# Kernel tuning notes

Hardware: AMD Instinct MI355X
Metric: run time of the kernel (lower is better)

Reference implementation:

```python
import jax, jax.numpy as jnp
import numpy as np

EPS = 1e-5
N_HEAD = 8

def setup_inputs() -> dict:
    key = jax.random.key(0)
    ks = jax.random.split(key, 8)
    n, c, h, w = 8, 512, 64, 64
    feats_in = 512
    x = jax.random.normal(ks[0], (n, c, h, w), jnp.float32)
    cond = jax.random.normal(ks[1], (n, feats_in), jnp.float32)
    # AdaGN linear: feats_in -> 2*c
    W_ada = jax.random.normal(ks[2], (feats_in, 2 * c), jnp.float32) * (1.0 / np.sqrt(feats_in))
    b_ada = jnp.zeros((2 * c,), jnp.float32)
    # qkv 1x1 conv: c -> 3c
    W_qkv = jax.random.normal(ks[3], (3 * c, c), jnp.float32) * (1.0 / np.sqrt(c))
    b_qkv = jnp.zeros((3 * c,), jnp.float32)
    # out 1x1 conv: c -> c
    W_out = jax.random.normal(ks[4], (c, c), jnp.float32) * (1.0 / np.sqrt(c))
    b_out = jnp.zeros((c,), jnp.float32)
    return {"x": x, "cond": cond, "W_ada": W_ada, "b_ada": b_ada,
            "W_qkv": W_qkv, "b_qkv": b_qkv, "W_out": W_out, "b_out": b_out}

def reference(x, cond, W_ada, b_ada, W_qkv, b_qkv, W_out, b_out):
    n, c, h, w = x.shape
    nh = N_HEAD
    dh = c // nh
    s = h * w
    # AdaGN: GroupNorm with 1 group, no affine, then scale/shift from cond
    scales_shifts = cond @ W_ada + b_ada  # [n, 2c]
    scales, shifts = scales_shifts[:, :c], scales_shifts[:, c:]
    xf = x.reshape(n, -1)
    mean = xf.mean(axis=1, keepdims=True)
    var = xf.var(axis=1, keepdims=True)
    normed = ((xf - mean) * jax.lax.rsqrt(var + EPS)).reshape(n, c, h, w)
    normed = shifts[:, :, None, None] + normed * (scales[:, :, None, None] + 1.0)
    # qkv 1x1 conv
    qkv = jnp.einsum('nchw,oc->nohw', normed, W_qkv) + b_qkv[None, :, None, None]
    # view [n, nh*3, dh, s] then transpose -> [n, nh*3, s, dh]
    qkv = qkv.reshape(n, nh * 3, dh, s).transpose(0, 1, 3, 2)
    q, k, v = jnp.split(qkv, 3, axis=1)  # each [n, nh, s, dh]
    scale = dh ** (-0.25)
    att = jnp.einsum('nhsd,nhtd->nhst', q * scale, k * scale)
    att = jax.nn.softmax(att, axis=-1)
    y = jnp.einsum('nhst,nhtd->nhsd', att, v)  # [n, nh, s, dh]
    y = y.transpose(0, 1, 3, 2).reshape(n, c, h, w)
    out = jnp.einsum('nchw,oc->nohw', y, W_out) + b_out[None, :, None, None]
    return x + out
```

## Files before the change

### kernel.cpp

```cpp
#include <hip/hip_runtime.h>

#define NB   8
#define CC   512
#define SS   4096
#define NHD  8
#define DH   64
#define FEAT 512
#define NPER (CC*SS)

typedef unsigned short ushort_t;
typedef __attribute__((ext_vector_type(8))) short bf16x8;
typedef __attribute__((ext_vector_type(4))) float f32x4;

__device__ inline float b2f(ushort_t h) {
    union { unsigned int u; float f; } v; v.u = ((unsigned int)h) << 16; return v.f;
}
__device__ inline ushort_t f2b(float f) {
    union { float f; unsigned int u; } v; v.f = f;
    unsigned int u = v.u;
    u += 0x7fffu + ((u >> 16) & 1u);
    return (ushort_t)(u >> 16);
}
__device__ inline void unpack8(uint4 v, ushort_t* us) {
    us[0] = v.x & 0xffff; us[1] = v.x >> 16;
    us[2] = v.y & 0xffff; us[3] = v.y >> 16;
    us[4] = v.z & 0xffff; us[5] = v.z >> 16;
    us[6] = v.w & 0xffff; us[7] = v.w >> 16;
}
__device__ inline float loadIn(const void* p, size_t idx, int isf) {
    return isf ? ((const float*)p)[idx] : b2f(((const ushort_t*)p)[idx]);
}
__device__ inline void load8(const void* p, size_t idx, int isf, float* f) {
    if (isf) {
        const float* q = (const float*)p + idx;
        float4 a = *(const float4*)q, b = *(const float4*)(q + 4);
        f[0]=a.x; f[1]=a.y; f[2]=a.z; f[3]=a.w; f[4]=b.x; f[5]=b.y; f[6]=b.z; f[7]=b.w;
    } else {
        uint4 v = *(const uint4*)((const ushort_t*)p + idx);
        ushort_t us[8]; unpack8(v, us);
        for (int j = 0; j < 8; ++j) f[j] = b2f(us[j]);
    }
}
__device__ inline bf16x8 loadfrag(const void* p, size_t idx, int isf) {
    if (isf) {
        float f[8]; load8(p, idx, 1, f);
        bf16x8 r;
        for (int j = 0; j < 8; ++j) r[j] = (short)f2b(f[j]);
        return r;
    }
    union { uint4 u; bf16x8 v; } cvt;
    cvt.u = *(const uint4*)((const ushort_t*)p + idx);
    return cvt.v;
}

typedef __attribute__((address_space(1))) const unsigned int gas_u32;
typedef __attribute__((address_space(3))) unsigned int las_u32;
__device__ inline void gload_lds16(const void* g, void* l) {
    __builtin_amdgcn_global_load_lds((gas_u32*)g, (las_u32*)l, 16, 0, 0);
}

__global__ void probe_kernel(const unsigned int* __restrict__ x, int* __restrict__ flag) {
    unsigned int w = x[threadIdx.x & 63];
    unsigned int elo = (w >> 7) & 0xFF;
    int hit = (elo >= 0x60 && elo <= 0x9F) ? 1 : 0;
    for (int m = 1; m < 64; m <<= 1) hit += __shfl_xor(hit, m, 64);
    if (threadIdx.x == 0) *flag = (hit >= 40) ? 0 : 1;
}

__global__ __launch_bounds__(256) void ada_kernel(
    const void* __restrict__ cond, const void* __restrict__ W,
    const void* __restrict__ bias, float* __restrict__ out,
    const int* __restrict__ flagp)
{
    int isf = *flagp;
    int n = blockIdx.x;
    int j = blockIdx.y * 256 + threadIdx.x;
    float acc = loadIn(bias, j, isf);
    for (int k = 0; k < FEAT; ++k)
        acc += loadIn(cond, (size_t)n * FEAT + k, isf) * loadIn(W, (size_t)k * (2 * CC) + j, isf);
    out[n * (2 * CC) + j] = acc;
}

__global__ __launch_bounds__(256) void stats_kernel(
    const void* __restrict__ x, float* __restrict__ part, const int* __restrict__ flagp)
{
    int isf = *flagp;
    int n = blockIdx.x, blk = blockIdx.y;
    int tid = threadIdx.x;
    float s = 0.f, ss = 0.f;
    size_t base8 = (size_t)blk * 4096 + tid;
    for (int i = 0; i < 16; ++i) {
        float f[8];
        load8(x, ((size_t)n * NPER) + (base8 + (size_t)i * 256) * 8, isf, f);
        for (int j = 0; j < 8; ++j) { s += f[j]; ss += f[j] * f[j]; }
    }
    for (int m = 1; m < 64; m <<= 1) { s += __shfl_xor(s, m, 64); ss += __shfl_xor(ss, m, 64); }
    int w = tid >> 6;
    if ((tid & 63) == 0) {
        part[(size_t)n * 512 + (blk * 4 + w) * 2 + 0] = s;
        part[(size_t)n * 512 + (blk * 4 + w) * 2 + 1] = ss;
    }
}

__global__ __launch_bounds__(256) void coef_kernel(
    const float* __restrict__ ada, const float* __restrict__ part,
    float* __restrict__ coefA, float* __restrict__ coefB)
{
    __shared__ float reds[4], redss[4], mv[2];
    int n = blockIdx.x;
    int tid = threadIdx.x;
    float s  = part[(size_t)n * 512 + tid * 2 + 0];
    float ss = part[(size_t)n * 512 + tid * 2 + 1];
    for (int m = 1; m < 64; m <<= 1) { s += __shfl_xor(s, m, 64); ss += __shfl_xor(ss, m, 64); }
    int w = tid >> 6, lane = tid & 63;
    if (lane == 0) { reds[w] = s; redss[w] = ss; }
    __syncthreads();
    if (tid == 0) {
        float S  = (reds[0] + reds[1]) + (reds[2] + reds[3]);
        float S2 = (redss[0] + redss[1]) + (redss[2] + redss[3]);
        float inv = 1.f / (float)NPER;
        float mean = S * inv;
        float var  = S2 * inv - mean * mean;
        mv[0] = mean;
        mv[1] = rsqrtf(var + 1e-5f);
    }
    __syncthreads();
    float mean = mv[0], r = mv[1];
    int c = blockIdx.y * 256 + tid;
    float a = (ada[n * (2 * CC) + c] + 1.f) * r;
    coefA[n * CC + c] = a;
    coefB[n * CC + c] = ada[n * (2 * CC) + CC + c] - mean * a;
}

__global__ __launch_bounds__(256) void qkv_gemm_kernel(
    const void* __restrict__ A, const void* __restrict__ X, const void* __restrict__ bias,
    ushort_t* __restrict__ C,
    const float* __restrict__ coefA, const float* __restrict__ coefB,
    const int* __restrict__ flagp, int nb, int hb, int hc)
{
    __shared__ __align__(16) short Alds[64][72];
    __shared__ __align__(16) short Blds[64][72];
    int isf = *flagp;
    int z = blockIdx.z;
    int nIdx = nb + z;
    int yb = blockIdx.y;
    int p = yb / hc, hh = yb % hc;
    int arow0 = p * 512 + (hb + hh) * 64;
    size_t cbase = ((size_t)(z * 3 + p) * (hc * 64) + hh * 64) * SS;
    int n0 = blockIdx.x * 64;
    int tid = threadIdx.x;
    int w = tid >> 6, lane = tid & 63;
    int quad = lane >> 4, l16 = lane & 15;
    int wm = (w >> 1) * 32, wn = (w & 1) * 32;
    f32x4 acc[2][2] = {};

    for (int k0 = 0; k0 < 512; k0 += 64) {
        __syncthreads();
        for (int it = 0; it < 2; ++it) {
            int chunk = tid + it * 256;
            int row = chunk >> 3, cb = chunk & 7;
            float f[8];
            load8(A, (size_t)(arow0 + row) * 512 + k0 + cb * 8, isf, f);
            short o[8];
            for (int j = 0; j < 8; ++j) o[j] = (short)f2b(f[j]);
            *(uint4*)&Alds[row][cb * 8] = *(uint4*)o;
        }
        for (int it = 0; it < 2; ++it) {
            int chunk = tid + it * 256;
            int c = chunk >> 3, hb8 = chunk & 7;
            int ch = k0 + c;
            float f[8];
            load8(X, (size_t)nIdx * NPER + (size_t)ch * SS + n0 + hb8 * 8, isf, f);
            float a = coefA[nIdx * CC + ch], b = coefB[nIdx * CC + ch];
            for (int j = 0; j < 8; ++j)
                Blds[hb8 * 8 + j][c] = (short)f2b(a * f[j] + b);
        }
        __syncthreads();
        for (int kk = 0; kk < 2; ++kk) {
            bf16x8 af[2], bfv[2];
            for (int mi = 0; mi < 2; ++mi)
                af[mi] = *(const bf16x8*)&Alds[wm + mi * 16 + l16][kk * 32 + quad * 8];
            for (int ni = 0; ni < 2; ++ni)
                bfv[ni] = *(const bf16x8*)&Blds[wn + ni * 16 + l16][kk * 32 + quad * 8];
            for (int mi = 0; mi < 2; ++mi)
                for (int ni = 0; ni < 2; ++ni)
                    acc[mi][ni] = __builtin_amdgcn_mfma_f32_16x16x32_bf16(
                        af[mi], bfv[ni], acc[mi][ni], 0, 0, 0);
        }
    }
    if (p < 2) {
        const float SCL = 0.42467078f;
        for (int mi = 0; mi < 2; ++mi)
            for (int ni = 0; ni < 2; ++ni) {
                int col = n0 + wn + ni * 16 + l16;
                int d0 = wm + mi * 16 + quad * 4;
                ushort_t pk[4];
                for (int r = 0; r < 4; ++r) {
                    float v = (acc[mi][ni][r] + loadIn(bias, arow0 + d0 + r, isf)) * SCL;
                    pk[r] = f2b(v);
                }
                *(ushort4*)&C[cbase + (size_t)col * 64 + d0] =
                    make_ushort4(pk[0], pk[1], pk[2], pk[3]);
            }
    } else {
        for (int mi = 0; mi < 2; ++mi)
            for (int ni = 0; ni < 2; ++ni) {
                int col = n0 + wn + ni * 16 + l16;
                for (int r = 0; r < 4; ++r) {
                    int rowl = wm + mi * 16 + quad * 4 + r;
                    float v = acc[mi][ni][r] + loadIn(bias, arow0 + rowl, isf);
                    C[cbase + (size_t)rowl * SS + col] = f2b(v);
                }
            }
    }
}

__global__ __launch_bounds__(256, 4) void attn_kernel(
    const ushort_t* __restrict__ qkv,
    ushort_t* __restrict__ y,
    int nb, int hb, int hc)
{
    __shared__ __align__(16) short Klds[2][64][64];
    __shared__ __align__(16) short Vlds[2][64][64];

    int s0 = blockIdx.x * 128;
    int hl = blockIdx.y;
    int z = blockIdx.z;
    int n = nb + z;
    int hcc = hc * 64;
    const ushort_t* Q = qkv + ((size_t)(z * 3 + 0) * hcc + hl * 64) * SS;
    const ushort_t* K = qkv + ((size_t)(z * 3 + 1) * hcc + hl * 64) * SS;
    const ushort_t* V = qkv + ((size_t)(z * 3 + 2) * hcc + hl * 64) * SS;

    int tid = threadIdx.x;
    int w = tid >> 6, lane = tid & 63;
    int quad = lane >> 4, l16 = lane & 15;
    int sw = l16 & 7;

    bf16x8 qf[2][2];
    for (int si = 0; si < 2; ++si)
        for (int kk = 0; kk < 2; ++kk)
            qf[si][kk] = *(const bf16x8*)&Q[(size_t)(s0 + w * 32 + si * 16 + l16) * 64
                                            + kk * 32 + quad * 8];

    auto stage = [&](int b, int tt) {
        #pragma unroll
        for (int it = 0; it < 2; ++it) {
            int chunk = it * 256 + tid;
            int row = chunk >> 3;
            int ssl = (chunk & 7) ^ (row & 7);
            int cb0 = it * 256 + w * 64;
            gload_lds16(&K[(size_t)(tt + row) * 64 + ssl * 8], (short*)Klds[b] + cb0 * 8);
            gload_lds16(&V[(size_t)row * SS + tt + ssl * 8],   (short*)Vlds[b] + cb0 * 8);
        }
    };

    const short ONE = 0x3F80;
    bf16x8 ones = { ONE, ONE, ONE, ONE, ONE, ONE, ONE, ONE };

    f32x4 o[2][4] = {};
    f32x4 sum_acc[2] = {};

    stage(0, 0);

    for (int t0 = 0; t0 < SS; t0 += 64) {
        int cur = (t0 >> 6) & 1;
        __syncthreads();
        if (t0 + 64 < SS) stage(cur ^ 1, t0 + 64);

        for (int kk = 0; kk < 2; ++kk) {
            f32x4 sv[2][2];
            for (int ntl = 0; ntl < 2; ++ntl) {
                int nt = kk * 2 + ntl;
                bf16x8 kf0 = *(const bf16x8*)&Klds[cur][nt * 16 + l16][((0 * 4 + quad) ^ sw) * 8];
                bf16x8 kf1 = *(const bf16x8*)&Klds[cur][nt * 16 + l16][((1 * 4 + quad) ^ sw) * 8];
                for (int si = 0; si < 2; ++si) {
                    f32x4 a = { -16.f, -16.f, -16.f, -16.f };
                    a = __builtin_amdgcn_mfma_f32_16x16x32_bf16(kf0, qf[si][0], a, 0, 0, 0);
                    a = __builtin_amdgcn_mfma_f32_16x16x32_bf16(kf1, qf[si][1], a, 0, 0, 0);
                    sv[ntl][si] = a;
                }
            }

            bf16x8 vf[4];
            for (int dt = 0; dt < 4; ++dt)
                vf[dt] = *(const bf16x8*)&Vlds[cur][dt * 16 + l16][((kk * 4 + quad) ^ sw) * 8];

            for (int si = 0; si < 2; ++si) {
                float p0 = exp2f(sv[0][si][0]), p1 = exp2f(sv[0][si][1]);
                float p2 = exp2f(sv[0][si][2]), p3 = exp2f(sv[0][si][3]);
                float p4 = exp2f(sv[1][si][0]), p5 = exp2f(sv[1][si][1]);
                float p6 = exp2f(sv[1][si][2]), p7 = exp2f(sv[1][si][3]);
                unsigned int x0, x1, y0, y1;
                asm("v_cvt_pk_bf16_f32 %0, %1, %2" : "=v"(x0) : "v"(p0), "v"(p1));
                asm("v_cvt_pk_bf16_f32 %0, %1, %2" : "=v"(x1) : "v"(p2), "v"(p3));
                asm("v_cvt_pk_bf16_f32 %0, %1, %2" : "=v"(y0) : "v"(p4), "v"(p5));
                asm("v_cvt_pk_bf16_f32 %0, %1, %2" : "=v"(y1) : "v"(p6), "v"(p7));
                asm("v_permlane32_swap_b32 %0, %1" : "+v"(x0), "+v"(y0));
                asm("v_permlane32_swap_b32 %0, %1" : "+v"(x1), "+v"(y1));
                asm("v_permlane16_swap_b32 %0, %1" : "+v"(x0), "+v"(y0));
                asm("v_permlane16_swap_b32 %0, %1" : "+v"(x1), "+v"(y1));
                union { unsigned int u[4]; bf16x8 v; } frag;
                frag.u[0] = x0; frag.u[1] = x1; frag.u[2] = y0; frag.u[3] = y1;

                sum_acc[si] = __builtin_amdgcn_mfma_f32_16x16x32_bf16(frag.v, ones, sum_acc[si], 0, 0, 0);
                for (int dt = 0; dt < 4; ++dt)
                    o[si][dt] = __builtin_amdgcn_mfma_f32_16x16x32_bf16(frag.v, vf[dt], o[si][dt], 0, 0, 0);
            }
        }
    }

    for (int si = 0; si < 2; ++si) {
        f32x4 inv;
        for (int r = 0; r < 4; ++r) inv[r] = 1.0f / sum_acc[si][r];
        for (int dt = 0; dt < 4; ++dt) {
            int d = dt * 16 + l16;
            int cidx = (hb + hl) * DH + d;
            size_t bidx = ((size_t)n * CC + cidx) * SS + s0 + w * 32 + si * 16 + quad * 4;
            ushort_t pk[4];
            for (int r = 0; r < 4; ++r) pk[r] = f2b(o[si][dt][r] * inv[r]);
            *(ushort4*)&y[bidx] = make_ushort4(pk[0], pk[1], pk[2], pk[3]);
        }
    }
}

__global__ __launch_bounds__(512) void out_gemm_kernel(
    const void* __restrict__ W, const void* __restrict__ bias, const void* __restrict__ x,
    const ushort_t* __restrict__ ybuf, float* __restrict__ out,
    const int* __restrict__ flagp)
{
    __shared__ __align__(16) short Ylds[64][264];
    int isf = *flagp;
    int n = blockIdx.y;
    int s0 = blockIdx.x * 64;
    int tid = threadIdx.x;
    int w = tid >> 6, lane = tid & 63;
    int quad = lane >> 4, l16 = lane & 15;
    const ushort_t* Yb = ybuf + (size_t)n * ((size_t)CC * SS);
    float* Op = out + (size_t)n * NPER;

    f32x4 acc[4][4] = {};
    for (int kh = 0; kh < 2; ++kh) {
        __syncthreads();
        int ch = (tid & 255) + kh * 256;
        int cg = tid >> 8;
        for (int cb = 0; cb < 4; ++cb) {
            uint4 v = *(const uint4*)&Yb[(size_t)ch * SS + s0 + cg * 32 + cb * 8];
            ushort_t us[8]; unpack8(v, us);
            for (int j = 0; j < 8; ++j) Ylds[cg * 32 + cb * 8 + j][tid & 255] = (short)us[j];
        }
        __syncthreads();
        for (int k0 = 0; k0 < 256; k0 += 32) {
            bf16x8 af[4];
            for (int mi = 0; mi < 4; ++mi)
                af[mi] = loadfrag(W, (size_t)(w * 64 + mi * 16 + l16) * 512 + kh * 256 + k0 + quad * 8, isf);
            for (int ni = 0; ni < 4; ++ni) {
                bf16x8 bfv = *(const bf16x8*)&Ylds[ni * 16 + l16][k0 + quad * 8];
                for (int mi = 0; mi < 4; ++mi)
                    acc[mi][ni] = __builtin_amdgcn_mfma_f32_16x16x32_bf16(
                        af[mi], bfv, acc[mi][ni], 0, 0, 0);
            }
        }
    }

    for (int mi = 0; mi < 4; ++mi)
        for (int ni = 0; ni < 4; ++ni) {
            int col = s0 + ni * 16 + l16;
            for (int r = 0; r < 4; ++r) {
                int m = w * 64 + mi * 16 + quad * 4 + r;
                size_t idx = (size_t)m * SS + col;
                float v = acc[mi][ni][r] + loadIn(bias, m, isf)
                        + loadIn(x, (size_t)n * NPER + idx, isf);
                Op[idx] = v;
            }
        }
}

extern "C" void kernel_launch(void* const* d_in, const int* in_sizes, int n_in,
                              void* d_out, int out_size, void* d_ws, size_t ws_size,
                              hipStream_t stream) {
    (void)in_sizes; (void)n_in; (void)out_size;
    const void* x     = d_in[0];
    const void* cond  = d_in[1];
    const void* W_ada = d_in[2];
    const void* b_ada = d_in[3];
    const void* W_qkv = d_in[4];
    const void* b_qkv = d_in[5];
    const void* W_out = d_in[6];
    const void* b_out = d_in[7];
    float* out = (float*)d_out;

    char* ws = (char*)d_ws;
    float* part  = (float*)ws;
    float* ada   = (float*)(ws + 16384);
    float* coefA = (float*)(ws + 49152);
    float* coefB = (float*)(ws + 65536);
    int*   flag  = (int*)(ws + 81920);
    ushort_t* ybuf   = (ushort_t*)(ws + 82176);
    const size_t BASE = 82176ULL + (size_t)NB * NPER * 2;
    ushort_t* qkvbuf = (ushort_t*)(ws + BASE);

    const size_t PER_HS = (size_t)3 * 64 * SS * 2;
    size_t avail = ws_size > BASE ? ws_size - BASE : 0;
    int NC = 1, HC = 1;
    if      (avail >= 64 * PER_HS) { NC = 8; HC = 8; }
    else if (avail >= 32 * PER_HS) { NC = 4; HC = 8; }
    else if (avail >= 16 * PER_HS) { NC = 2; HC = 8; }
    else if (avail >=  8 * PER_HS) { NC = 1; HC = 8; }
    else if (avail >=  4 * PER_HS) { NC = 1; HC = 4; }
    else if (avail >=  2 * PER_HS) { NC = 1; HC = 2; }

    probe_kernel<<<1, 64, 0, stream>>>((const unsigned int*)x, flag);
    ada_kernel  <<<dim3(NB, 4),  256, 0, stream>>>(cond, W_ada, b_ada, ada, flag);
    stats_kernel<<<dim3(NB, 64), 256, 0, stream>>>(x, part, flag);
    coef_kernel <<<dim3(NB, 2),  256, 0, stream>>>(ada, part, coefA, coefB);

    for (int nb = 0; nb < NB; nb += NC)
        for (int hb = 0; hb < NHD; hb += HC) {
            qkv_gemm_kernel<<<dim3(64, 3 * HC, NC), 256, 0, stream>>>(
                W_qkv, x, b_qkv, qkvbuf, coefA, coefB, flag, nb, hb, HC);
            attn_kernel<<<dim3(32, HC, NC), 256, 0, stream>>>(
                qkvbuf, ybuf, nb, hb, HC);
        }

    out_gemm_kernel<<<dim3(64, NB), 512, 0, stream>>>(W_out, b_out, x, ybuf, out, flag);
}
```

Before: 916.8 us.

## Fold AdaGN scale/shift into per-batch QKV weights and pre-convert weights to bf16

The AdaGN affine normalization is folded algebraically into a per-sample scaled QKV weight matrix (W*a) and adjusted bias (b + W·b'), computed once by a new kernel. The QKV GEMM then loads bf16 weights directly into LDS through async global-to-LDS loads with an XOR swizzle, and no longer applies the per-channel normalization to X. W_out is also pre-converted to bf16 once, so the output GEMM loads it directly. These steps remove per-tile conversion and FMA work at the cost of extra prep kernels and about 12.5MB of additional workspace, and the wprime kernel has poor memory coalescing (one thread per output row, striding by 512).

```diff
diff --git a/kernel.cpp b/kernel.cpp
--- a/kernel.cpp
+++ b/kernel.cpp
@@ -40,17 +40,6 @@
         ushort_t us[8]; unpack8(v, us);
         for (int j = 0; j < 8; ++j) f[j] = b2f(us[j]);
     }
-}
-__device__ inline bf16x8 loadfrag(const void* p, size_t idx, int isf) {
-    if (isf) {
-        float f[8]; load8(p, idx, 1, f);
-        bf16x8 r;
-        for (int j = 0; j < 8; ++j) r[j] = (short)f2b(f[j]);
-        return r;
-    }
-    union { uint4 u; bf16x8 v; } cvt;
-    cvt.u = *(const uint4*)((const ushort_t*)p + idx);
-    return cvt.v;
 }
 
 typedef __attribute__((address_space(1))) const unsigned int gas_u32;
@@ -132,13 +121,56 @@
     coefB[n * CC + c] = ada[n * (2 * CC) + CC + c] - mean * a;
 }
 
+__global__ __launch_bounds__(256) void wprime_kernel(
+    const void* __restrict__ W, const void* __restrict__ bias,
+    const float* __restrict__ coefA, const float* __restrict__ coefB,
+    ushort_t* __restrict__ Wp, float* __restrict__ bias2,
+    const int* __restrict__ flagp)
+{
+    int isf = *flagp;
+    int n = blockIdx.x;
+    int o = blockIdx.y * 256 + threadIdx.x;
+    const float* cA = coefA + n * CC;
+    const float* cB = coefB + n * CC;
+    float bacc = loadIn(bias, o, isf);
+    ushort_t* dst = Wp + ((size_t)n * 1536 + o) * 512;
+    for (int c = 0; c < 512; c += 8) {
+        float wv[8];
+        load8(W, (size_t)o * 512 + c, isf, wv);
+        float4 a0 = *(const float4*)&cA[c], a1 = *(const float4*)&cA[c + 4];
+        float4 b0 = *(const float4*)&cB[c], b1 = *(const float4*)&cB[c + 4];
+        float av[8] = {a0.x, a0.y, a0.z, a0.w, a1.x, a1.y, a1.z, a1.w};
+        float bv[8] = {b0.x, b0.y, b0.z, b0.w, b1.x, b1.y, b1.z, b1.w};
+        ushort_t pk[8];
+        for (int j = 0; j < 8; ++j) {
+            bacc += wv[j] * bv[j];
+            pk[j] = f2b(wv[j] * av[j]);
+        }
+        *(ushort4*)&dst[c]     = make_ushort4(pk[0], pk[1], pk[2], pk[3]);
+        *(ushort4*)&dst[c + 4] = make_ushort4(pk[4], pk[5], pk[6], pk[7]);
+    }
+    bias2[n * 1536 + o] = bacc;
+}
+
+__global__ __launch_bounds__(256) void wconv_kernel(
+    const void* __restrict__ W, ushort_t* __restrict__ Wb, const int* __restrict__ flagp)
+{
+    int isf = *flagp;
+    size_t i = ((size_t)blockIdx.x * 256 + threadIdx.x) * 8;
+    float f[8];
+    load8(W, i, isf, f);
+    ushort_t pk[8];
+    for (int j = 0; j < 8; ++j) pk[j] = f2b(f[j]);
+    *(ushort4*)&Wb[i]     = make_ushort4(pk[0], pk[1], pk[2], pk[3]);
+    *(ushort4*)&Wb[i + 4] = make_ushort4(pk[4], pk[5], pk[6], pk[7]);
+}
+
 __global__ __launch_bounds__(256) void qkv_gemm_kernel(
-    const void* __restrict__ A, const void* __restrict__ X, const void* __restrict__ bias,
-    ushort_t* __restrict__ C,
-    const float* __restrict__ coefA, const float* __restrict__ coefB,
+    const ushort_t* __restrict__ Wp, const void* __restrict__ X,
+    const float* __restrict__ bias2, ushort_t* __restrict__ C,
     const int* __restrict__ flagp, int nb, int hb, int hc)
 {
-    __shared__ __align__(16) short Alds[64][72];
+    __shared__ __align__(16) short Alds[64][64];
     __shared__ __align__(16) short Blds[64][72];
     int isf = *flagp;
     int z = blockIdx.z;
@@ -152,34 +184,33 @@
     int w = tid >> 6, lane = tid & 63;
     int quad = lane >> 4, l16 = lane & 15;
     int wm = (w >> 1) * 32, wn = (w & 1) * 32;
+    const ushort_t* Arow = Wp + ((size_t)nIdx * 1536 + arow0) * 512;
     f32x4 acc[2][2] = {};
 
     for (int k0 = 0; k0 < 512; k0 += 64) {
         __syncthreads();
         for (int it = 0; it < 2; ++it) {
-            int chunk = tid + it * 256;
-            int row = chunk >> 3, cb = chunk & 7;
-            float f[8];
-            load8(A, (size_t)(arow0 + row) * 512 + k0 + cb * 8, isf, f);
-            short o[8];
-            for (int j = 0; j < 8; ++j) o[j] = (short)f2b(f[j]);
-            *(uint4*)&Alds[row][cb * 8] = *(uint4*)o;
+            int chunk = it * 256 + tid;
+            int row = chunk >> 3;
+            int ssl = (chunk & 7) ^ (row & 7);
+            int cb0 = it * 256 + w * 64;
+            gload_lds16(&Arow[(size_t)row * 512 + k0 + ssl * 8], (short*)Alds + cb0 * 8);
         }
         for (int it = 0; it < 2; ++it) {
             int chunk = tid + it * 256;
-            int c = chunk >> 3, hb8 = chunk & 7;
-            int ch = k0 + c;
+            int cc = chunk >> 3, hb8 = chunk & 7;
+            int ch = k0 + cc;
             float f[8];
             load8(X, (size_t)nIdx * NPER + (size_t)ch * SS + n0 + hb8 * 8, isf, f);
-            float a = coefA[nIdx * CC + ch], b = coefB[nIdx * CC + ch];
             for (int j = 0; j < 8; ++j)
-                Blds[hb8 * 8 + j][c] = (short)f2b(a * f[j] + b);
+                Blds[hb8 * 8 + j][cc] = (short)f2b(f[j]);
         }
         __syncthreads();
         for (int kk = 0; kk < 2; ++kk) {
             bf16x8 af[2], bfv[2];
             for (int mi = 0; mi < 2; ++mi)
-                af[mi] = *(const bf16x8*)&Alds[wm + mi * 16 + l16][kk * 32 + quad * 8];
+                af[mi] = *(const bf16x8*)&Alds[wm + mi * 16 + l16]
+                                              [((kk * 4 + quad) ^ (l16 & 7)) * 8];
             for (int ni = 0; ni < 2; ++ni)
                 bfv[ni] = *(const bf16x8*)&Blds[wn + ni * 16 + l16][kk * 32 + quad * 8];
             for (int mi = 0; mi < 2; ++mi)
@@ -188,6 +219,7 @@
                         af[mi], bfv[ni], acc[mi][ni], 0, 0, 0);
         }
     }
+    const float* b2p = bias2 + (size_t)nIdx * 1536;
     if (p < 2) {
         const float SCL = 0.42467078f;
         for (int mi = 0; mi < 2; ++mi)
@@ -196,7 +228,7 @@
                 int d0 = wm + mi * 16 + quad * 4;
                 ushort_t pk[4];
                 for (int r = 0; r < 4; ++r) {
-                    float v = (acc[mi][ni][r] + loadIn(bias, arow0 + d0 + r, isf)) * SCL;
+                    float v = (acc[mi][ni][r] + b2p[arow0 + d0 + r]) * SCL;
                     pk[r] = f2b(v);
                 }
                 *(ushort4*)&C[cbase + (size_t)col * 64 + d0] =
@@ -208,7 +240,7 @@
                 int col = n0 + wn + ni * 16 + l16;
                 for (int r = 0; r < 4; ++r) {
                     int rowl = wm + mi * 16 + quad * 4 + r;
-                    float v = acc[mi][ni][r] + loadIn(bias, arow0 + rowl, isf);
+                    float v = acc[mi][ni][r] + b2p[arow0 + rowl];
                     C[cbase + (size_t)rowl * SS + col] = f2b(v);
                 }
             }
@@ -325,7 +357,7 @@
 }
 
 __global__ __launch_bounds__(512) void out_gemm_kernel(
-    const void* __restrict__ W, const void* __restrict__ bias, const void* __restrict__ x,
+    const ushort_t* __restrict__ Wb, const void* __restrict__ bias, const void* __restrict__ x,
     const ushort_t* __restrict__ ybuf, float* __restrict__ out,
     const int* __restrict__ flagp)
 {
@@ -353,7 +385,8 @@
         for (int k0 = 0; k0 < 256; k0 += 32) {
             bf16x8 af[4];
             for (int mi = 0; mi < 4; ++mi)
-                af[mi] = loadfrag(W, (size_t)(w * 64 + mi * 16 + l16) * 512 + kh * 256 + k0 + quad * 8, isf);
+                af[mi] = *(const bf16x8*)&Wb[(size_t)(w * 64 + mi * 16 + l16) * 512
+                                             + kh * 256 + k0 + quad * 8];
             for (int ni = 0; ni < 4; ++ni) {
                 bf16x8 bfv = *(const bf16x8*)&Ylds[ni * 16 + l16][k0 + quad * 8];
                 for (int mi = 0; mi < 4; ++mi)
@@ -391,13 +424,16 @@
     float* out = (float*)d_out;
 
     char* ws = (char*)d_ws;
-    float* part  = (float*)ws;
-    float* ada   = (float*)(ws + 16384);
-    float* coefA = (float*)(ws + 49152);
-    float* coefB = (float*)(ws + 65536);
-    int*   flag  = (int*)(ws + 81920);
-    ushort_t* ybuf   = (ushort_t*)(ws + 82176);
-    const size_t BASE = 82176ULL + (size_t)NB * NPER * 2;
+    float* part   = (float*)ws;
+    float* ada    = (float*)(ws + 16384);
+    float* coefA  = (float*)(ws + 49152);
+    float* coefB  = (float*)(ws + 65536);
+    int*   flag   = (int*)(ws + 81920);
+    ushort_t* woutb  = (ushort_t*)(ws + 82176);
+    float* bias2  = (float*)(ws + 606464);
+    ushort_t* wprime = (ushort_t*)(ws + 655616);
+    ushort_t* ybuf   = (ushort_t*)(ws + 13238528);
+    const size_t BASE = 13238528ULL + (size_t)NB * NPER * 2;
     ushort_t* qkvbuf = (ushort_t*)(ws + BASE);
 
     const size_t PER_HS = (size_t)3 * 64 * SS * 2;
@@ -410,18 +446,20 @@
     else if (avail >=  4 * PER_HS) { NC = 1; HC = 4; }
     else if (avail >=  2 * PER_HS) { NC = 1; HC = 2; }
 
-    probe_kernel<<<1, 64, 0, stream>>>((const unsigned int*)x, flag);
-    ada_kernel  <<<dim3(NB, 4),  256, 0, stream>>>(cond, W_ada, b_ada, ada, flag);
-    stats_kernel<<<dim3(NB, 64), 256, 0, stream>>>(x, part, flag);
-    coef_kernel <<<dim3(NB, 2),  256, 0, stream>>>(ada, part, coefA, coefB);
+    probe_kernel <<<1, 64, 0, stream>>>((const unsigned int*)x, flag);
+    ada_kernel   <<<dim3(NB, 4),  256, 0, stream>>>(cond, W_ada, b_ada, ada, flag);
+    stats_kernel <<<dim3(NB, 64), 256, 0, stream>>>(x, part, flag);
+    coef_kernel  <<<dim3(NB, 2),  256, 0, stream>>>(ada, part, coefA, coefB);
+    wprime_kernel<<<dim3(NB, 6),  256, 0, stream>>>(W_qkv, b_qkv, coefA, coefB, wprime, bias2, flag);
+    wconv_kernel <<<dim3(128),    256, 0, stream>>>(W_out, woutb, flag);
 
     for (int nb = 0; nb < NB; nb += NC)
         for (int hb = 0; hb < NHD; hb += HC) {
             qkv_gemm_kernel<<<dim3(64, 3 * HC, NC), 256, 0, stream>>>(
-                W_qkv, x, b_qkv, qkvbuf, coefA, coefB, flag, nb, hb, HC);
+                wprime, x, bias2, qkvbuf, flag, nb, hb, HC);
             attn_kernel<<<dim3(32, HC, NC), 256, 0, stream>>>(
                 qkvbuf, ybuf, nb, hb, HC);
         }
 
-    out_gemm_kernel<<<dim3(64, NB), 512, 0, stream>>>(W_out, b_out, x, ybuf, out, flag);
-}
+    out_gemm_kernel<<<dim3(64, NB), 512, 0, stream>>>(woutb, b_out, x, ybuf, out, flag);
+}
```

Result: no change. 909.4 us (-0.8%).
